# Kernel tuning notes

Measured on AMD Instinct MI355X. Metric: run time of the kernel, lower is better.

The kernel has to match this reference:

```python
import jax, jax.numpy as jnp
import numpy as np

H = 1024          # hidden_size
M = 512           # moe_intermediate_size
E = 16            # num_routed_experts
TOP_K = 2         # num_experts_per_tok
SCALE = 2.5       # routed_scaling_factor
NORM_TOPK = True  # norm_topk_prob
B, S = 1, 1024


def setup_inputs() -> dict:
    key = jax.random.key(0)
    ks = jax.random.split(key, 8)
    std = 0.02
    return {
        "hidden_states": jax.random.normal(ks[0], (B, S, H), jnp.float32),
        "gate_w": jax.random.normal(ks[1], (E, H), jnp.float32) * std,
        "w_gate": jax.random.normal(ks[2], (E, H, M), jnp.float32) * std,
        "w_up": jax.random.normal(ks[3], (E, H, M), jnp.float32) * std,
        "w_down": jax.random.normal(ks[4], (E, M, H), jnp.float32) * std,
        "ws_gate": jax.random.normal(ks[5], (H, M), jnp.float32) * std,
        "ws_up": jax.random.normal(ks[6], (H, M), jnp.float32) * std,
        "ws_down": jax.random.normal(ks[7], (M, H), jnp.float32) * std,
    }


def _moe(x, gate_w, w_gate, w_up, w_down, ws_gate, ws_up, ws_down):
    # x: [T, H] flattened tokens
    T = x.shape[0]
    # shared expert (SwiGLU): down(silu(gate(x)) * up(x))
    shared = (jax.nn.silu(x @ ws_gate) * (x @ ws_up)) @ ws_down  # [T, H]

    # sigmoid gating in fp32 (matches F.linear on fp32 + sigmoid)
    scores = jax.nn.sigmoid(x.astype(jnp.float32) @ gate_w.T.astype(jnp.float32))  # [T, E]
    topk_w, topk_idx = jax.lax.top_k(scores, TOP_K)  # [T, K]
    if NORM_TOPK and TOP_K > 1:
        topk_w = topk_w / (topk_w.sum(-1, keepdims=True) + 1e-20)
    topk_w = topk_w * SCALE

    # dense combine weights [T, E]; zero for non-selected experts, so weighting
    # all-expert outputs is mathematically identical to the dispatch/gather path
    route = jnp.zeros((T, E), topk_w.dtype).at[jnp.arange(T)[:, None], topk_idx].set(topk_w)

    # per-expert SwiGLU over all tokens (grouped-GEMM reference)
    g = jnp.einsum("th,ehm->etm", x, w_gate)                 # [E, T, M]
    u = jnp.einsum("th,ehm->etm", x, w_up)                   # [E, T, M]
    eo = jnp.einsum("etm,emh->eth", jax.nn.silu(g) * u, w_down)  # [E, T, H]
    routed = jnp.einsum("te,eth->th", route.astype(x.dtype), eo)  # [T, H]
    return routed + shared


def reference(hidden_states, gate_w, w_gate, w_up, w_down, ws_gate, ws_up, ws_down):
    b, s, h = hidden_states.shape
    x = hidden_states.reshape(-1, h)
    out = _moe(x, gate_w, w_gate, w_up, w_down, ws_gate, ws_up, ws_down)
    return out.reshape(b, s, h)
```

## Files before the change

kernel.cpp:

```cpp
#include <hip/hip_runtime.h>
#include <math.h>

#define TT 1024
#define HH 1024
#define MM 512
#define NE 16

typedef _Float16 f16;
typedef _Float16 f16x8 __attribute__((ext_vector_type(8)));
typedef float f32x4 __attribute__((ext_vector_type(4)));

#define GLL(g, l) __builtin_amdgcn_global_load_lds(                         \
    (const __attribute__((address_space(1))) void*)(g),                     \
    (__attribute__((address_space(3))) void*)(l), 16, 0, 0)

#define SB() __builtin_amdgcn_sched_barrier(0)
#define WAITVM(N) { SB(); asm volatile("s_waitcnt vmcnt(" #N ")"); SB(); }
#define BARRIER() __builtin_amdgcn_s_barrier()

__global__ __launch_bounds__(256) void router_k(
    const float* __restrict__ x, const float* __restrict__ gate_w,
    int* __restrict__ counts, int* __restrict__ token_list, float* __restrict__ weight_list)
{
    const int wave = threadIdx.x >> 6;
    const int lane = threadIdx.x & 63;
    const int t = (blockIdx.x << 2) + wave;
    const float* xr = x + (size_t)t * HH;
    float xv[16];
#pragma unroll
    for (int i = 0; i < 16; ++i) xv[i] = xr[lane + (i << 6)];
    float sc[NE];
#pragma unroll
    for (int e = 0; e < NE; ++e) {
        const float* gr = gate_w + e * HH;
        float acc = 0.f;
#pragma unroll
        for (int i = 0; i < 16; ++i) acc = fmaf(xv[i], gr[lane + (i << 6)], acc);
#pragma unroll
        for (int off = 32; off > 0; off >>= 1) acc += __shfl_down(acc, off, 64);
        sc[e] = acc;
    }
    if (lane == 0) {
        float l1 = -1e30f, l2 = -1e30f; int i1 = 0, i2 = 0;
#pragma unroll
        for (int e = 0; e < NE; ++e) {
            float v = sc[e];
            if (v > l1) { l2 = l1; i2 = i1; l1 = v; i1 = e; }
            else if (v > l2) { l2 = v; i2 = e; }
        }
        float w1 = 1.f / (1.f + __expf(-l1));
        float w2 = 1.f / (1.f + __expf(-l2));
        const float inv = 2.5f / (w1 + w2 + 1e-20f);
        w1 *= inv; w2 *= inv;
        int s1 = atomicAdd(&counts[i1], 1);
        token_list[i1 * TT + s1] = t;
        weight_list[i1 * TT + s1] = w1;
        int s2 = atomicAdd(&counts[i2], 1);
        token_list[i2 * TT + s2] = t;
        weight_list[i2 * TT + s2] = w2;
    }
}

__global__ void prefix_k(const int* __restrict__ counts, int* __restrict__ offs)
{
    if (threadIdx.x == 0 && blockIdx.x == 0) {
        int acc = 0;
#pragma unroll
        for (int e = 0; e < NE; ++e) { offs[e] = acc; acc += counts[e]; }
        offs[NE] = acc;
    }
}


#define GU_ISSUE(K0, AS, BG, BU) {                                          \
    _Pragma("unroll") for (int i = 0; i < 4; ++i)                           \
        GLL(pA[i] + (K0), &AS[aw + 4*i][0]);                                \
    _Pragma("unroll") for (int i = 0; i < 2; ++i) {                         \
        GLL(pBg[i] + (size_t)(K0) * MM, &BG[(w << 4) + 8*i][0]);            \
        GLL(pBu[i] + (size_t)(K0) * MM, &BU[(w << 4) + 8*i][0]); } }

#define GU_COMP(AS, BG, BU) {                                               \
    _Pragma("unroll") for (int h = 0; h < 2; ++h) {                         \
        const int kb = (h << 5) + (lg << 3);                                \
        const int xr = (lm & 7) << 2;                                       \
        f16x8 af[2];                                                        \
        _Pragma("unroll") for (int f = 0; f < 2; ++f) {                     \
            const int m = wm + (f << 4) + lm;                               \
            float4 lo = *(const float4*)&AS[m][kb ^ xr];                    \
            float4 hi = *(const float4*)&AS[m][(kb + 4) ^ xr];              \
            af[f] = (f16x8){(f16)lo.x,(f16)lo.y,(f16)lo.z,(f16)lo.w,        \
                            (f16)hi.x,(f16)hi.y,(f16)hi.z,(f16)hi.w};       \
        }                                                                   \
        const int bc = (wn + lm) ^ ((lg & 1) << 4);                         \
        f16x8 bg, bu;                                                       \
        _Pragma("unroll") for (int j = 0; j < 8; ++j) {                     \
            bg[j] = (f16)BG[kb + j][bc]; bu[j] = (f16)BU[kb + j][bc]; }     \
        _Pragma("unroll") for (int f = 0; f < 2; ++f) {                     \
            accg[f] = __builtin_amdgcn_mfma_f32_16x16x32_f16(af[f], bg, accg[f], 0, 0, 0); \
            accu[f] = __builtin_amdgcn_mfma_f32_16x16x32_f16(af[f], bu, accu[f], 0, 0, 0); } } }

__global__ __launch_bounds__(256) void gu_k(
    const float* __restrict__ x,
    const float* __restrict__ w_gate, const float* __restrict__ w_up,
    const float* __restrict__ ws_gate, const float* __restrict__ ws_up,
    const int* __restrict__ counts, const int* __restrict__ offs,
    const int* __restrict__ token_list, f16* __restrict__ rinter)
{
    const int F = blockIdx.x;
    const int Q = F & 7;
    const int J = F >> 3;
    int e, tile;
    if (J < 512) { e = Q + ((J >> 8) << 3); tile = J & 255; }
    else         { e = NE; tile = (Q << 5) + (J - 512); }
    const int n0 = (tile & 15) << 5;
    const int r0 = (tile >> 4) << 6;

    int cnt, slot0;
    const float *wgp, *wup;
    if (e < NE) {
        cnt = counts[e]; slot0 = offs[e];
        wgp = w_gate + (size_t)e * HH * MM;
        wup = w_up   + (size_t)e * HH * MM;
    } else {
        cnt = TT; slot0 = 2 * TT;
        wgp = ws_gate; wup = ws_up;
    }
    if (r0 >= cnt) return;

    __shared__ float As0[64][64], As1[64][64];
    __shared__ float Bg0[64][32], Bg1[64][32];
    __shared__ float Bu0[64][32], Bu1[64][32];
    __shared__ int toks[64];

    const int tid = threadIdx.x;
    if (tid < 64) {
        int i = r0 + tid; if (i >= cnt) i = cnt - 1;
        toks[tid] = (e < NE) ? token_list[e * TT + i] : i;
    }
    __syncthreads();

    const int w = tid >> 6, lane = tid & 63;
    const int lm = lane & 15, lg = lane >> 4;
    const int wm = (w >> 1) << 5, wn = (w & 1) << 4;
    const int aw = w << 4;

    const float* pA[4];
#pragma unroll
    for (int i = 0; i < 4; ++i) {
        int m = aw + 4*i + (lane >> 4);
        pA[i] = x + (size_t)toks[m] * HH + 4 * ((lane & 15) ^ (m & 7));
    }
    const float* pBg[2]; const float* pBu[2];
#pragma unroll
    for (int i = 0; i < 2; ++i) {
        int kr = (w << 4) + 8*i + (lane >> 3);
        int sg = 4 * ((lane & 7) ^ ((i & 1) << 2));
        pBg[i] = wgp + (size_t)kr * MM + n0 + sg;
        pBu[i] = wup + (size_t)kr * MM + n0 + sg;
    }

    f32x4 accg[2] = {}, accu[2] = {};

    GU_ISSUE(0, As0, Bg0, Bu0)
#pragma unroll 1
    for (int t = 0; t < 14; t += 2) {
        GU_ISSUE((t + 1) << 6, As1, Bg1, Bu1)
        WAITVM(8) BARRIER();
        GU_COMP(As0, Bg0, Bu0)
        BARRIER();
        GU_ISSUE((t + 2) << 6, As0, Bg0, Bu0)
        WAITVM(8) BARRIER();
        GU_COMP(As1, Bg1, Bu1)
        BARRIER();
    }
    GU_ISSUE(15 << 6, As1, Bg1, Bu1)
    WAITVM(8) BARRIER();
    GU_COMP(As0, Bg0, Bu0)
    BARRIER();
    WAITVM(0) BARRIER();
    GU_COMP(As1, Bg1, Bu1)

#pragma unroll
    for (int fi = 0; fi < 2; ++fi)
#pragma unroll
        for (int rr = 0; rr < 4; ++rr) {
            const int m = wm + (fi << 4) + (lg << 2) + rr;
            if (r0 + m < cnt) {
                float g = accg[fi][rr], u = accu[fi][rr];
                float s = g / (1.f + __expf(-g));
                rinter[(size_t)(slot0 + r0 + m) * MM + n0 + wn + lm] = (f16)(s * u);
            }
        }
}


#define DN_ISSUE(K0, AS, BS) {                                              \
    _Pragma("unroll") for (int i = 0; i < 2; ++i) {                         \
        GLL(pa[i] + (K0), &AS[(w << 4) + 8*i][0]);                          \
        GLL(pb[i] + (size_t)(K0) * HH, &BS[(w << 4) + 8*i][0]); } }

#define DN_COMP(AS, BS) {                                                   \
    _Pragma("unroll") for (int h = 0; h < 2; ++h) {                         \
        const int kb = (h << 5) + (lg << 3);                                \
        const int xr = (lm & 7) << 3;                                       \
        f16x8 af[2];                                                        \
        _Pragma("unroll") for (int f = 0; f < 2; ++f)                       \
            af[f] = *(const f16x8*)&AS[wm + (f << 4) + lm][kb ^ xr];        \
        const int bc = (wn + lm) ^ ((lg & 1) << 4);                         \
        f16x8 bv;                                                           \
        _Pragma("unroll") for (int j = 0; j < 8; ++j) bv[j] = (f16)BS[kb + j][bc]; \
        _Pragma("unroll") for (int f = 0; f < 2; ++f)                       \
            acc[f] = __builtin_amdgcn_mfma_f32_16x16x32_f16(af[f], bv, acc[f], 0, 0, 0); } }

__global__ __launch_bounds__(256) void down_k(
    const f16* __restrict__ rinter,
    const float* __restrict__ w_down, const float* __restrict__ ws_down,
    const int* __restrict__ counts, const int* __restrict__ offs,
    const int* __restrict__ token_list, const float* __restrict__ weight_list,
    float* __restrict__ out)
{
    const int F = blockIdx.x;
    const int Q = F & 7;
    const int J = F >> 3;
    int e, tile;
    if (J < 1024) { e = Q + ((J >> 9) << 3); tile = J & 511; }
    else          { e = NE; tile = (Q << 6) + (J - 1024); }
    const int n0 = (tile & 31) << 5;
    const int r0 = (tile >> 5) << 6;

    int cnt, slot0; const float* wdp;
    if (e < NE) { cnt = counts[e]; slot0 = offs[e]; wdp = w_down + (size_t)e * MM * HH; }
    else        { cnt = TT; slot0 = 2 * TT; wdp = ws_down; }
    if (r0 >= cnt) return;

    __shared__ f16  As0[64][64], As1[64][64];
    __shared__ float Bs0[64][32], Bs1[64][32];

    const int tid = threadIdx.x;
    const int w = tid >> 6, lane = tid & 63;
    const int lm = lane & 15, lg = lane >> 4;
    const int wm = (w >> 1) << 5, wn = (w & 1) << 4;

    const f16* pa[2]; const float* pb[2];
#pragma unroll
    for (int i = 0; i < 2; ++i) {
        int m = (w << 4) + 8*i + (lane >> 3);
        pa[i] = rinter + (size_t)(slot0 + r0 + m) * MM + 8 * ((lane & 7) ^ (m & 7));
        int kr = (w << 4) + 8*i + (lane >> 3);
        pb[i] = wdp + (size_t)kr * HH + n0 + 4 * ((lane & 7) ^ ((i & 1) << 2));
    }

    f32x4 acc[2] = {};

    DN_ISSUE(0, As0, Bs0)
#pragma unroll 1
    for (int t = 0; t < 6; t += 2) {
        DN_ISSUE((t + 1) << 6, As1, Bs1)
        WAITVM(4) BARRIER();
        DN_COMP(As0, Bs0)
        BARRIER();
        DN_ISSUE((t + 2) << 6, As0, Bs0)
        WAITVM(4) BARRIER();
        DN_COMP(As1, Bs1)
        BARRIER();
    }
    DN_ISSUE(7 << 6, As1, Bs1)
    WAITVM(4) BARRIER();
    DN_COMP(As0, Bs0)
    BARRIER();
    WAITVM(0) BARRIER();
    DN_COMP(As1, Bs1)

#pragma unroll
    for (int fi = 0; fi < 2; ++fi)
#pragma unroll
        for (int rr = 0; rr < 4; ++rr) {
            const int m = wm + (fi << 4) + (lg << 2) + rr;
            const int row = r0 + m;
            if (row < cnt) {
                int t; float wt;
                if (e < NE) { t = token_list[e * TT + row]; wt = weight_list[e * TT + row]; }
                else        { t = row; wt = 1.f; }
                atomicAdd(&out[(size_t)t * HH + n0 + wn + lm], wt * acc[fi][rr]);
            }
        }
}

extern "C" void kernel_launch(void* const* d_in, const int* in_sizes, int n_in,
                              void* d_out, int out_size, void* d_ws, size_t ws_size,
                              hipStream_t stream)
{
    const float* x       = (const float*)d_in[0];
    const float* gate_w  = (const float*)d_in[1];
    const float* w_gate  = (const float*)d_in[2];
    const float* w_up    = (const float*)d_in[3];
    const float* w_down  = (const float*)d_in[4];
    const float* ws_gate = (const float*)d_in[5];
    const float* ws_up   = (const float*)d_in[6];
    const float* ws_down = (const float*)d_in[7];
    float* out = (float*)d_out;

    int* counts = (int*)d_ws;
    int* offs = counts + 16;
    int* token_list = counts + 64;
    float* weight_list = (float*)(counts + 64 + NE * TT);
    f16* rinter = (f16*)(counts + 64 + 2 * NE * TT);

    hipMemsetAsync(counts, 0, 64, stream);
    hipMemsetAsync(out, 0, (size_t)TT * HH * sizeof(float), stream);
    router_k<<<dim3(TT / 4), 256, 0, stream>>>(x, gate_w, counts, token_list, weight_list);
    prefix_k<<<1, 64, 0, stream>>>(counts, offs);
    gu_k<<<dim3(8 * 544), 256, 0, stream>>>(
        x, w_gate, w_up, ws_gate, ws_up, counts, offs, token_list, rinter);
    down_k<<<dim3(8 * 1088), 256, 0, stream>>>(
        rinter, w_down, ws_down, counts, offs, token_list, weight_list, out);
}
```

Before: 105.5 us.

## Load A fragments directly to registers from fp16 x and triple-buffer B tiles

Adds a pack kernel that converts x to fp16 once. The gate/up kernel then reads A operands straight from global memory into registers in MFMA fragment layout, and the down kernel does the same for its intermediate, so A no longer goes through LDS. Weight tiles move to a three-stage LDS ring with a single barrier per K-step, which removes the second barrier per step and the per-step fp32-to-fp16 conversion of A. In exchange it adds an extra kernel launch and a pass over x, raises register pressure, and issues non-coalesced direct register loads.

```diff
diff --git a/kernel.cpp b/kernel.cpp
--- a/kernel.cpp
+++ b/kernel.cpp
@@ -7,16 +7,24 @@
 #define NE 16
 
 typedef _Float16 f16;
+typedef _Float16 f16x4 __attribute__((ext_vector_type(4)));
 typedef _Float16 f16x8 __attribute__((ext_vector_type(8)));
 typedef float f32x4 __attribute__((ext_vector_type(4)));
 
 #define GLL(g, l) __builtin_amdgcn_global_load_lds(                         \
     (const __attribute__((address_space(1))) void*)(g),                     \
     (__attribute__((address_space(3))) void*)(l), 16, 0, 0)
-
 #define SB() __builtin_amdgcn_sched_barrier(0)
 #define WAITVM(N) { SB(); asm volatile("s_waitcnt vmcnt(" #N ")"); SB(); }
 #define BARRIER() __builtin_amdgcn_s_barrier()
+
+__global__ __launch_bounds__(256) void pack_k(const float* __restrict__ x, f16* __restrict__ xh)
+{
+    const int i = (blockIdx.x * 256 + threadIdx.x) * 4;
+    float4 v = *(const float4*)(x + i);
+    f16x4 h = { (f16)v.x, (f16)v.y, (f16)v.z, (f16)v.w };
+    *(f16x4*)(xh + i) = h;
+}
 
 __global__ __launch_bounds__(256) void router_k(
     const float* __restrict__ x, const float* __restrict__ gate_w,
@@ -72,35 +80,39 @@
 }
 
 
-#define GU_ISSUE(K0, AS, BG, BU) {                                          \
-    _Pragma("unroll") for (int i = 0; i < 4; ++i)                           \
-        GLL(pA[i] + (K0), &AS[aw + 4*i][0]);                                \
+#define GU_ALOAD(SL, T2) {                                                  \
+    aA##SL##_[0] = *(const f16x8*)(pa0 + ((T2) << 6));                      \
+    aA##SL##_[1] = *(const f16x8*)(pa0 + ((T2) << 6) + 32);                 \
+    aA##SL##_[2] = *(const f16x8*)(pa1 + ((T2) << 6));                      \
+    aA##SL##_[3] = *(const f16x8*)(pa1 + ((T2) << 6) + 32); }
+
+#define GU_BISSUE(K0, BG, BU) {                                             \
     _Pragma("unroll") for (int i = 0; i < 2; ++i) {                         \
         GLL(pBg[i] + (size_t)(K0) * MM, &BG[(w << 4) + 8*i][0]);            \
         GLL(pBu[i] + (size_t)(K0) * MM, &BU[(w << 4) + 8*i][0]); } }
 
-#define GU_COMP(AS, BG, BU) {                                               \
+#define GU_COMP(SU, BG, BU) {                                               \
     _Pragma("unroll") for (int h = 0; h < 2; ++h) {                         \
         const int kb = (h << 5) + (lg << 3);                                \
-        const int xr = (lm & 7) << 2;                                       \
-        f16x8 af[2];                                                        \
-        _Pragma("unroll") for (int f = 0; f < 2; ++f) {                     \
-            const int m = wm + (f << 4) + lm;                               \
-            float4 lo = *(const float4*)&AS[m][kb ^ xr];                    \
-            float4 hi = *(const float4*)&AS[m][(kb + 4) ^ xr];              \
-            af[f] = (f16x8){(f16)lo.x,(f16)lo.y,(f16)lo.z,(f16)lo.w,        \
-                            (f16)hi.x,(f16)hi.y,(f16)hi.z,(f16)hi.w};       \
-        }                                                                   \
         const int bc = (wn + lm) ^ ((lg & 1) << 4);                         \
         f16x8 bg, bu;                                                       \
         _Pragma("unroll") for (int j = 0; j < 8; ++j) {                     \
             bg[j] = (f16)BG[kb + j][bc]; bu[j] = (f16)BU[kb + j][bc]; }     \
         _Pragma("unroll") for (int f = 0; f < 2; ++f) {                     \
-            accg[f] = __builtin_amdgcn_mfma_f32_16x16x32_f16(af[f], bg, accg[f], 0, 0, 0); \
-            accu[f] = __builtin_amdgcn_mfma_f32_16x16x32_f16(af[f], bu, accu[f], 0, 0, 0); } } }
+            accg[f] = __builtin_amdgcn_mfma_f32_16x16x32_f16(aA##SU##_[2*f+h], bg, accg[f], 0, 0, 0); \
+            accu[f] = __builtin_amdgcn_mfma_f32_16x16x32_f16(aA##SU##_[2*f+h], bu, accu[f], 0, 0, 0); } } }
+
+#define GU_PH(T, SU, SL, VC) {                                              \
+    WAITVM(VC)                                                              \
+    BARRIER();                                                              \
+    if ((T) + 2 < 16) {                                                     \
+        GU_ALOAD(SL, (T)+2)                                                 \
+        GU_BISSUE(((T)+2) << 6, Bg##SL, Bu##SL)                             \
+    }                                                                       \
+    GU_COMP(SU, Bg##SU, Bu##SU) }
 
 __global__ __launch_bounds__(256) void gu_k(
-    const float* __restrict__ x,
+    const f16* __restrict__ xh,
     const float* __restrict__ w_gate, const float* __restrict__ w_up,
     const float* __restrict__ ws_gate, const float* __restrict__ ws_up,
     const int* __restrict__ counts, const int* __restrict__ offs,
@@ -127,9 +139,8 @@
     }
     if (r0 >= cnt) return;
 
-    __shared__ float As0[64][64], As1[64][64];
-    __shared__ float Bg0[64][32], Bg1[64][32];
-    __shared__ float Bu0[64][32], Bu1[64][32];
+    __shared__ float Bg0[64][32], Bg1[64][32], Bg2[64][32];
+    __shared__ float Bu0[64][32], Bu1[64][32], Bu2[64][32];
     __shared__ int toks[64];
 
     const int tid = threadIdx.x;
@@ -142,14 +153,10 @@
     const int w = tid >> 6, lane = tid & 63;
     const int lm = lane & 15, lg = lane >> 4;
     const int wm = (w >> 1) << 5, wn = (w & 1) << 4;
-    const int aw = w << 4;
-
-    const float* pA[4];
-#pragma unroll
-    for (int i = 0; i < 4; ++i) {
-        int m = aw + 4*i + (lane >> 4);
-        pA[i] = x + (size_t)toks[m] * HH + 4 * ((lane & 15) ^ (m & 7));
-    }
+
+    const f16* pa0 = xh + (size_t)toks[wm + lm]      * HH + (lg << 3);
+    const f16* pa1 = xh + (size_t)toks[wm + 16 + lm] * HH + (lg << 3);
+
     const float* pBg[2]; const float* pBu[2];
 #pragma unroll
     for (int i = 0; i < 2; ++i) {
@@ -160,25 +167,15 @@
     }
 
     f32x4 accg[2] = {}, accu[2] = {};
-
-    GU_ISSUE(0, As0, Bg0, Bu0)
-#pragma unroll 1
-    for (int t = 0; t < 14; t += 2) {
-        GU_ISSUE((t + 1) << 6, As1, Bg1, Bu1)
-        WAITVM(8) BARRIER();
-        GU_COMP(As0, Bg0, Bu0)
-        BARRIER();
-        GU_ISSUE((t + 2) << 6, As0, Bg0, Bu0)
-        WAITVM(8) BARRIER();
-        GU_COMP(As1, Bg1, Bu1)
-        BARRIER();
-    }
-    GU_ISSUE(15 << 6, As1, Bg1, Bu1)
-    WAITVM(8) BARRIER();
-    GU_COMP(As0, Bg0, Bu0)
-    BARRIER();
-    WAITVM(0) BARRIER();
-    GU_COMP(As1, Bg1, Bu1)
+    f16x8 aA0_[4], aA1_[4], aA2_[4];
+
+    GU_ALOAD(0, 0) GU_BISSUE(0, Bg0, Bu0)
+    GU_ALOAD(1, 1) GU_BISSUE(1 << 6, Bg1, Bu1)
+
+    GU_PH(0, 0, 2, 4)  GU_PH(1, 1, 0, 4)  GU_PH(2, 2, 1, 4)  GU_PH(3, 0, 2, 4)
+    GU_PH(4, 1, 0, 4)  GU_PH(5, 2, 1, 4)  GU_PH(6, 0, 2, 4)  GU_PH(7, 1, 0, 4)
+    GU_PH(8, 2, 1, 4)  GU_PH(9, 0, 2, 4)  GU_PH(10, 1, 0, 4) GU_PH(11, 2, 1, 4)
+    GU_PH(12, 0, 2, 4) GU_PH(13, 1, 0, 4) GU_PH(14, 2, 1, 4) GU_PH(15, 0, 2, 0)
 
 #pragma unroll
     for (int fi = 0; fi < 2; ++fi)
@@ -194,23 +191,33 @@
 }
 
 
-#define DN_ISSUE(K0, AS, BS) {                                              \
-    _Pragma("unroll") for (int i = 0; i < 2; ++i) {                         \
-        GLL(pa[i] + (K0), &AS[(w << 4) + 8*i][0]);                          \
-        GLL(pb[i] + (size_t)(K0) * HH, &BS[(w << 4) + 8*i][0]); } }
-
-#define DN_COMP(AS, BS) {                                                   \
+#define DN_ALOAD(SL, T2) {                                                  \
+    aD##SL##_[0] = *(const f16x8*)(pa0 + ((T2) << 6));                      \
+    aD##SL##_[1] = *(const f16x8*)(pa0 + ((T2) << 6) + 32);                 \
+    aD##SL##_[2] = *(const f16x8*)(pa1 + ((T2) << 6));                      \
+    aD##SL##_[3] = *(const f16x8*)(pa1 + ((T2) << 6) + 32); }
+
+#define DN_BISSUE(K0, BS) {                                                 \
+    _Pragma("unroll") for (int i = 0; i < 2; ++i)                           \
+        GLL(pb[i] + (size_t)(K0) * HH, &BS[(w << 4) + 8*i][0]); }
+
+#define DN_COMP(SU, BS) {                                                   \
     _Pragma("unroll") for (int h = 0; h < 2; ++h) {                         \
         const int kb = (h << 5) + (lg << 3);                                \
-        const int xr = (lm & 7) << 3;                                       \
-        f16x8 af[2];                                                        \
-        _Pragma("unroll") for (int f = 0; f < 2; ++f)                       \
-            af[f] = *(const f16x8*)&AS[wm + (f << 4) + lm][kb ^ xr];        \
         const int bc = (wn + lm) ^ ((lg & 1) << 4);                         \
         f16x8 bv;                                                           \
         _Pragma("unroll") for (int j = 0; j < 8; ++j) bv[j] = (f16)BS[kb + j][bc]; \
         _Pragma("unroll") for (int f = 0; f < 2; ++f)                       \
-            acc[f] = __builtin_amdgcn_mfma_f32_16x16x32_f16(af[f], bv, acc[f], 0, 0, 0); } }
+            acc[f] = __builtin_amdgcn_mfma_f32_16x16x32_f16(aD##SU##_[2*f+h], bv, acc[f], 0, 0, 0); } }
+
+#define DN_PH(T, SU, SL, VC) {                                              \
+    WAITVM(VC)                                                              \
+    BARRIER();                                                              \
+    if ((T) + 2 < 8) {                                                      \
+        DN_ALOAD(SL, (T)+2)                                                 \
+        DN_BISSUE(((T)+2) << 6, Bs##SL)                                     \
+    }                                                                       \
+    DN_COMP(SU, Bs##SU) }
 
 __global__ __launch_bounds__(256) void down_k(
     const f16* __restrict__ rinter,
@@ -233,43 +240,31 @@
     else        { cnt = TT; slot0 = 2 * TT; wdp = ws_down; }
     if (r0 >= cnt) return;
 
-    __shared__ f16  As0[64][64], As1[64][64];
-    __shared__ float Bs0[64][32], Bs1[64][32];
+    __shared__ float Bs0[64][32], Bs1[64][32], Bs2[64][32];
 
     const int tid = threadIdx.x;
     const int w = tid >> 6, lane = tid & 63;
     const int lm = lane & 15, lg = lane >> 4;
     const int wm = (w >> 1) << 5, wn = (w & 1) << 4;
 
-    const f16* pa[2]; const float* pb[2];
+    const f16* pa0 = rinter + (size_t)(slot0 + r0 + wm + lm)      * MM + (lg << 3);
+    const f16* pa1 = rinter + (size_t)(slot0 + r0 + wm + 16 + lm) * MM + (lg << 3);
+
+    const float* pb[2];
 #pragma unroll
     for (int i = 0; i < 2; ++i) {
-        int m = (w << 4) + 8*i + (lane >> 3);
-        pa[i] = rinter + (size_t)(slot0 + r0 + m) * MM + 8 * ((lane & 7) ^ (m & 7));
         int kr = (w << 4) + 8*i + (lane >> 3);
         pb[i] = wdp + (size_t)kr * HH + n0 + 4 * ((lane & 7) ^ ((i & 1) << 2));
     }
 
     f32x4 acc[2] = {};
-
-    DN_ISSUE(0, As0, Bs0)
-#pragma unroll 1
-    for (int t = 0; t < 6; t += 2) {
-        DN_ISSUE((t + 1) << 6, As1, Bs1)
-        WAITVM(4) BARRIER();
-        DN_COMP(As0, Bs0)
-        BARRIER();
-        DN_ISSUE((t + 2) << 6, As0, Bs0)
-        WAITVM(4) BARRIER();
-        DN_COMP(As1, Bs1)
-        BARRIER();
-    }
-    DN_ISSUE(7 << 6, As1, Bs1)
-    WAITVM(4) BARRIER();
-    DN_COMP(As0, Bs0)
-    BARRIER();
-    WAITVM(0) BARRIER();
-    DN_COMP(As1, Bs1)
+    f16x8 aD0_[4], aD1_[4], aD2_[4];
+
+    DN_ALOAD(0, 0) DN_BISSUE(0, Bs0)
+    DN_ALOAD(1, 1) DN_BISSUE(1 << 6, Bs1)
+
+    DN_PH(0, 0, 2, 2) DN_PH(1, 1, 0, 2) DN_PH(2, 2, 1, 2) DN_PH(3, 0, 2, 2)
+    DN_PH(4, 1, 0, 2) DN_PH(5, 2, 1, 2) DN_PH(6, 0, 2, 2) DN_PH(7, 1, 0, 0)
 
 #pragma unroll
     for (int fi = 0; fi < 2; ++fi)
@@ -305,13 +300,15 @@
     int* token_list = counts + 64;
     float* weight_list = (float*)(counts + 64 + NE * TT);
     f16* rinter = (f16*)(counts + 64 + 2 * NE * TT);
+    f16* xh = rinter + (size_t)3072 * MM;
 
     hipMemsetAsync(counts, 0, 64, stream);
     hipMemsetAsync(out, 0, (size_t)TT * HH * sizeof(float), stream);
+    pack_k<<<dim3(TT * HH / 1024), 256, 0, stream>>>(x, xh);
     router_k<<<dim3(TT / 4), 256, 0, stream>>>(x, gate_w, counts, token_list, weight_list);
     prefix_k<<<1, 64, 0, stream>>>(counts, offs);
     gu_k<<<dim3(8 * 544), 256, 0, stream>>>(
-        x, w_gate, w_up, ws_gate, ws_up, counts, offs, token_list, rinter);
+        xh, w_gate, w_up, ws_gate, ws_up, counts, offs, token_list, rinter);
     down_k<<<dim3(8 * 1088), 256, 0, stream>>>(
         rinter, w_down, ws_down, counts, offs, token_list, weight_list, out);
 }
```

Result: slower. 136.9 us (+29.7%).
